# Kernel tuning notes

Measured on AMD Instinct MI355X. Metric: run time of the kernel, lower is better.

The kernel has to match this reference:

```python
import jax, jax.numpy as jnp
import numpy as np

D_MODEL = 1024
N_HEADS = 16
HEAD_DIM = 64
SEQ = 2048
BATCH = 2
NEG = -1e9


def rotate_half(t):
    t1, t2 = jnp.split(t, 2, axis=-1)
    return jnp.concatenate([-t2, t1], axis=-1)


def setup_inputs() -> dict:
    key = jax.random.key(0)
    ks = jax.random.split(key, 7)
    std = 0.02
    x = jax.random.normal(ks[0], (BATCH, SEQ, D_MODEL), dtype=jnp.float32)
    # RoPE tables [seq_len, head_dim]
    inv_freq = 1.0 / (10000.0 ** (jnp.arange(0, HEAD_DIM, 2, dtype=jnp.float32) / HEAD_DIM))
    t = jnp.arange(SEQ, dtype=jnp.float32)
    freqs = jnp.outer(t, inv_freq)
    emb = jnp.concatenate([freqs, freqs], axis=-1)
    cos = jnp.cos(emb)
    sin = jnp.sin(emb)
    Wq = std * jax.random.normal(ks[1], (D_MODEL, D_MODEL), dtype=jnp.float32)
    Wk = std * jax.random.normal(ks[2], (D_MODEL, D_MODEL), dtype=jnp.float32)
    Wv = std * jax.random.normal(ks[3], (D_MODEL, D_MODEL), dtype=jnp.float32)
    Wo = std * jax.random.normal(ks[4], (D_MODEL, D_MODEL), dtype=jnp.float32)
    return {"x": x, "cos": cos, "sin": sin, "Wq": Wq, "Wk": Wk, "Wv": Wv, "Wo": Wo}


def reference(x, cos, sin, Wq, Wk, Wv, Wo):
    B, S, _ = x.shape
    scale = 1.0 / np.sqrt(HEAD_DIM)
    # projections (nn.Linear: y = x @ W.T)
    q = (x @ Wq.T).reshape(B, S, N_HEADS, HEAD_DIM).transpose(0, 2, 1, 3)  # [B,H,S,D]
    k = (x @ Wk.T).reshape(B, S, N_HEADS, HEAD_DIM).transpose(0, 2, 1, 3)
    v = (x @ Wv.T).reshape(B, S, N_HEADS, HEAD_DIM).transpose(0, 2, 1, 3)
    # RoPE
    c = cos[None, None, :, :]
    s = sin[None, None, :, :]
    q = q * c + rotate_half(q) * s
    k = k * c + rotate_half(k) * s
    # attention with additive causal mask
    scores = jnp.einsum('bhqd,bhkd->bhqk', q, k) * scale
    causal = jnp.triu(jnp.ones((S, S), dtype=jnp.float32), k=1) * NEG
    scores = scores + causal[None, None]
    attn = jax.nn.softmax(scores, axis=-1)
    out = jnp.einsum('bhqk,bhkd->bhqd', attn, v)
    out = out.transpose(0, 2, 1, 3).reshape(B, S, D_MODEL)
    return out @ Wo.T
```

## Files before the change

### kernel.cpp

```cpp
#include <hip/hip_runtime.h>
#include <hip/hip_bf16.h>
#include <math.h>

#define DM    1024
#define SEQL  2048
#define NB    2
#define MTOT  4096

typedef __attribute__((ext_vector_type(8))) short short8;
typedef __attribute__((ext_vector_type(4))) short short4v;
typedef __attribute__((ext_vector_type(4))) float float4v;

#define GLDS16(g, l) __builtin_amdgcn_global_load_lds( \
    (const __attribute__((address_space(1))) void*)(g), \
    (__attribute__((address_space(3))) void*)(l), 16, 0, 0)

__device__ __forceinline__ short f2bf(float f) {
  union { float f; unsigned u; } c; c.f = f;
  unsigned r = c.u + 0x7FFFu + ((c.u >> 16) & 1u);
  return (short)(r >> 16);
}

__device__ __forceinline__ int packbf(float a, float b) {
  union { float f; unsigned u; } ca, cb; ca.f = a; cb.f = b;
  return (int)__builtin_amdgcn_perm(cb.u + 0x8000u, ca.u + 0x8000u, 0x07060302u);
}

__global__ __launch_bounds__(256) void cvt_all(
    const float* __restrict__ x, const float* __restrict__ wq, const float* __restrict__ wk,
    const float* __restrict__ wv, const float* __restrict__ wo,
    short* __restrict__ xb, short* __restrict__ wqb, short* __restrict__ wkb,
    short* __restrict__ wvb, short* __restrict__ wob) {
  const int n4x = MTOT * DM / 4;
  int i = blockIdx.x * 256 + threadIdx.x;
  const float* s; short* d; int off;
  if (i < n4x) { s = x; d = xb; off = i; }
  else {
    int j = i - n4x;
    int sel = j >> 18;
    off = j & 0x3FFFF;
    s = (sel == 0) ? wq : (sel == 1) ? wk : (sel == 2) ? wv : wo;
    d = (sel == 0) ? wqb : (sel == 1) ? wkb : (sel == 2) ? wvb : wob;
  }
  float4 v = ((const float4*)s)[off];
  short4v o;
  o.x = f2bf(v.x); o.y = f2bf(v.y); o.z = f2bf(v.z); o.w = f2bf(v.w);
  ((short4v*)d)[off] = o;
}

__global__ __launch_bounds__(256, 2) void qkv_kernel(
    const short* __restrict__ A,
    const short* __restrict__ B0, const short* __restrict__ B1, const short* __restrict__ B2,
    short* __restrict__ out0, short* __restrict__ out1, short* __restrict__ out2,
    const float* __restrict__ cosp, const float* __restrict__ sinp)
{
  __shared__ short As[3][128 * 32];
  __shared__ short Bs[3][3][64 * 32];
  const int t = threadIdx.x;
  const int w = t >> 6, lane = t & 63;
  const int quad = lane >> 4, l16 = lane & 15;
  const int bm = blockIdx.y * 128, bn = blockIdx.x * 64;

  const short* Bz[3] = { B0, B1, B2 };

  float4v acc[3][2][4];
#pragma unroll
  for (int z = 0; z < 3; ++z)
#pragma unroll
    for (int i = 0; i < 2; ++i)
#pragma unroll
      for (int j = 0; j < 4; ++j) { float4v zr = {0.f, 0.f, 0.f, 0.f}; acc[z][i][j] = zr; }

  auto stage = [&](int k0, int p) {
#pragma unroll
    for (int i = 0; i < 2; ++i) {
      const int s = i * 256 + t;
      const int row = s >> 2, kc = (s & 3) ^ (row & 3);
      GLDS16(A + (size_t)(bm + row) * DM + k0 + kc * 8, &As[p][(i * 256 + w * 64) * 8]);
    }
#pragma unroll
    for (int z = 0; z < 3; ++z) {
      const int row = t >> 2, kc = (t & 3) ^ (row & 3);
      GLDS16(Bz[z] + (size_t)(bn + row) * DM + k0 + kc * 8, &Bs[z][p][(w * 64) * 8]);
    }
  };

  stage(0, 0);
  stage(32, 1);
  for (int ki = 0; ki < 32; ++ki) {
    const int p = ki % 3;
    if (ki < 31) { asm volatile("s_waitcnt vmcnt(5)" ::: "memory"); }
    else         { asm volatile("s_waitcnt vmcnt(0)" ::: "memory"); }
    __builtin_amdgcn_s_barrier();
    __builtin_amdgcn_sched_barrier(0);
    if (ki + 2 < 32) stage((ki + 2) * 32, (ki + 2) % 3);

    short8 af[2], bf[3][4];
#pragma unroll
    for (int mt = 0; mt < 2; ++mt) {
      const int row = w * 32 + mt * 16 + l16;
      af[mt] = *(const short8*)&As[p][(row * 4 + (quad ^ (row & 3))) * 8];
    }
#pragma unroll
    for (int z = 0; z < 3; ++z)
#pragma unroll
      for (int nt = 0; nt < 4; ++nt) {
        const int row = nt * 16 + l16;
        bf[z][nt] = *(const short8*)&Bs[z][p][(row * 4 + (quad ^ (row & 3))) * 8];
      }
    __builtin_amdgcn_s_setprio(1);
#pragma unroll
    for (int z = 0; z < 3; ++z)
#pragma unroll
      for (int mt = 0; mt < 2; ++mt)
#pragma unroll
        for (int nt = 0; nt < 4; ++nt)
          acc[z][mt][nt] = __builtin_amdgcn_mfma_f32_16x16x32_bf16(
              af[mt], bf[z][nt], acc[z][mt][nt], 0, 0, 0);
    __builtin_amdgcn_s_setprio(0);
  }

#pragma unroll
  for (int z = 0; z < 2; ++z) {
    short* qo = (z == 0) ? out0 : out1;
    const float sc = (z == 0) ? 0.18033688011112042f : 1.0f;
#pragma unroll
    for (int mt = 0; mt < 2; ++mt)
#pragma unroll
      for (int r = 0; r < 4; ++r) {
        int grow = bm + w * 32 + mt * 16 + quad * 4 + r;
        int s = grow & (SEQL - 1);
        int base = grow * DM + bn;
#pragma unroll
        for (int nt = 0; nt < 2; ++nt) {
          int d1 = nt * 16 + l16;
          float q1 = acc[z][mt][nt][r], q2 = acc[z][mt][nt + 2][r];
          float c1 = cosp[s * 64 + d1] * sc,      s1 = sinp[s * 64 + d1] * sc;
          float c2 = cosp[s * 64 + 32 + d1] * sc, s2 = sinp[s * 64 + 32 + d1] * sc;
          qo[base + d1]      = f2bf(q1 * c1 - q2 * s1);
          qo[base + 32 + d1] = f2bf(q2 * c2 + q1 * s2);
        }
      }
  }
#pragma unroll
  for (int mt = 0; mt < 2; ++mt)
#pragma unroll
    for (int nt = 0; nt < 4; ++nt) {
      int gc = bn + nt * 16 + l16;
      int g0 = bm + w * 32 + mt * 16 + quad * 4;
      short4v pk;
#pragma unroll
      for (int r = 0; r < 4; ++r) pk[r] = f2bf(acc[2][mt][nt][r]);
      *(short4v*)&out2[(size_t)gc * MTOT + g0] = pk;
    }
}

__global__ __launch_bounds__(512, 4) void attn_kernel(
    const short* __restrict__ Q, const short* __restrict__ K,
    const short* __restrict__ Vt, short* __restrict__ O)
{
  __shared__ short smem[34816];
  short* Ks = smem;
  short* Vs = smem + 8192;
  const int t = threadIdx.x;
  const int wid = t >> 6, lane = t & 63;
  const int quad = lane >> 4, l16 = lane & 15;
  const int g = wid >> 2;
  const int qg = wid & 3;
  short* Pl = smem + 16384 + wid * (2 * 16 * 72);
  const int qtA = blockIdx.x, qtB = 31 - blockIdx.x;
  const int bh = blockIdx.y, b = bh >> 4, h = bh & 15;
  const int rowbase = b * SEQL, colbase = h * 64;
  const int nktA = (qtA >> 1) + 1, nktB = (qtB >> 1) + 1;
  const int qA = qtA * 64 + qg * 16 + l16;
  const int qB = qtB * 64 + qg * 16 + l16;

  short8 aqA[2], aqB[2];
#pragma unroll
  for (int kk = 0; kk < 2; ++kk) {
    aqA[kk] = *(const short8*)&Q[(size_t)(rowbase + qA) * DM + colbase + kk * 32 + quad * 8];
    aqB[kk] = *(const short8*)&Q[(size_t)(rowbase + qB) * DM + colbase + kk * 32 + quad * 8];
  }

  float4v oA[4], oB[4];
#pragma unroll
  for (int j = 0; j < 4; ++j) { float4v z = {0.f, 0.f, 0.f, 0.f}; oA[j] = z; oB[j] = z; }
  float lA = 0.f, lB = 0.f;

  const short* Kbase0 = K + (size_t)rowbase * DM + colbase;
  const short* Vbase0 = Vt + (size_t)colbase * MTOT + rowbase;

  auto stageK = [&](int kt) {
#pragma unroll
    for (int j = 0; j < 2; ++j) {
      int i = j * 512 + t;
      int n = i >> 3, c = (i & 7) ^ (n & 7);
      GLDS16(Kbase0 + (size_t)(kt * 128 + n) * DM + c * 8, Ks + (j * 512 + wid * 64) * 8);
    }
  };
  auto stageV = [&](int kt) {
#pragma unroll
    for (int j = 0; j < 2; ++j) {
      int i = j * 512 + t;
      int d = i >> 4, c = (i & 15) ^ (d & 7);
      GLDS16(Vbase0 + (size_t)d * MTOT + kt * 128 + c * 8, Vs + (j * 512 + wid * 64) * 8);
    }
  };

  stageK(0);
  stageV(0);
  for (int kt = 0; kt < nktB; ++kt) {
    asm volatile("s_waitcnt vmcnt(2)" ::: "memory");
    __builtin_amdgcn_s_barrier();
    __builtin_amdgcn_sched_barrier(0);

    const bool actA = (kt < nktA);
    const bool diagA = (kt == nktA - 1), diagB = (kt == nktB - 1);

#pragma unroll
    for (int ntl = 0; ntl < 4; ++ntl) {
      const int nt = g * 4 + ntl;
      const int n = nt * 16 + l16;
      short8 bk0 = *(const short8*)&Ks[(n * 8 + (quad ^ (n & 7))) * 8];
      short8 bk1 = *(const short8*)&Ks[(n * 8 + ((4 + quad) ^ (n & 7))) * 8];
      const int kb = kt * 128 + nt * 16 + quad * 4;
      float4v zz = {0.f, 0.f, 0.f, 0.f};
      __builtin_amdgcn_s_setprio(1);
      float4v sB = __builtin_amdgcn_mfma_f32_16x16x32_bf16(bk0, aqB[0], zz, 0, 0, 0);
      sB = __builtin_amdgcn_mfma_f32_16x16x32_bf16(bk1, aqB[1], sB, 0, 0, 0);
      float4v sA;
      if (actA) {
        sA = __builtin_amdgcn_mfma_f32_16x16x32_bf16(bk0, aqA[0], zz, 0, 0, 0);
        sA = __builtin_amdgcn_mfma_f32_16x16x32_bf16(bk1, aqA[1], sA, 0, 0, 0);
      }
      __builtin_amdgcn_s_setprio(0);
      float pb[4];
#pragma unroll
      for (int r = 0; r < 4; ++r) {
        float pv = (diagB && (kb + r > qB)) ? 0.f : __builtin_amdgcn_exp2f(sB[r]);
        lB += pv; pb[r] = pv;
      }
      *(int2*)&Pl[1 * 16 * 72 + l16 * 72 + ntl * 16 + quad * 4] =
          make_int2(packbf(pb[0], pb[1]), packbf(pb[2], pb[3]));
      if (actA) {
        float pa[4];
#pragma unroll
        for (int r = 0; r < 4; ++r) {
          float pv = (diagA && (kb + r > qA)) ? 0.f : __builtin_amdgcn_exp2f(sA[r]);
          lA += pv; pa[r] = pv;
        }
        *(int2*)&Pl[0 * 16 * 72 + l16 * 72 + ntl * 16 + quad * 4] =
            make_int2(packbf(pa[0], pa[1]), packbf(pa[2], pa[3]));
      }
    }

    asm volatile("s_waitcnt vmcnt(0)" ::: "memory");
    __builtin_amdgcn_s_barrier();
    __builtin_amdgcn_sched_barrier(0);

    if (kt + 1 < nktB) stageK(kt + 1);

#pragma unroll
    for (int kk = 0; kk < 2; ++kk) {
      short8 apB = *(const short8*)&Pl[1 * 16 * 72 + l16 * 72 + kk * 32 + quad * 8];
      short8 apA;
      if (actA) apA = *(const short8*)&Pl[0 * 16 * 72 + l16 * 72 + kk * 32 + quad * 8];
      const int c0 = g * 8 + kk * 4 + quad;
      __builtin_amdgcn_s_setprio(1);
#pragma unroll
      for (int dt = 0; dt < 4; ++dt) {
        const int d = dt * 16 + l16;
        short8 bv = *(const short8*)&Vs[(d * 16 + (c0 ^ (d & 7))) * 8];
        oB[dt] = __builtin_amdgcn_mfma_f32_16x16x32_bf16(apB, bv, oB[dt], 0, 0, 0);
        if (actA) oA[dt] = __builtin_amdgcn_mfma_f32_16x16x32_bf16(apA, bv, oA[dt], 0, 0, 0);
      }
      __builtin_amdgcn_s_setprio(0);
    }

    __builtin_amdgcn_s_barrier();
    __builtin_amdgcn_sched_barrier(0);

    if (kt + 1 < nktB) stageV(kt + 1);
  }

  lA += __shfl_xor(lA, 16); lA += __shfl_xor(lA, 32);
  lB += __shfl_xor(lB, 16); lB += __shfl_xor(lB, 32);

  __syncthreads();
  float* Ored = (float*)smem;
  float* Lred = (float*)smem + 8448;
  if (g == 1) {
#pragma unroll
    for (int tile = 0; tile < 2; ++tile) {
      const float4v* src = (tile == 0) ? oA : oB;
      const int base = ((tile * 4 + qg) * 16) * 66;
#pragma unroll
      for (int dt = 0; dt < 4; ++dt)
#pragma unroll
        for (int r = 0; r < 4; ++r)
          Ored[base + (quad * 4 + r) * 66 + dt * 16 + l16] = src[dt][r];
    }
    if (lane < 16) {
      Lred[(0 * 4 + qg) * 16 + l16] = lA;
      Lred[(1 * 4 + qg) * 16 + l16] = lB;
    }
  }
  __syncthreads();
  if (g == 0) {
    const float tA = lA + Lred[(0 * 4 + qg) * 16 + l16];
    const float tB = lB + Lred[(1 * 4 + qg) * 16 + l16];
    float iAr[4], iBr[4];
#pragma unroll
    for (int r = 0; r < 4; ++r) {
      iAr[r] = 1.f / __shfl(tA, quad * 4 + r);
      iBr[r] = 1.f / __shfl(tB, quad * 4 + r);
    }
#pragma unroll
    for (int tile = 0; tile < 2; ++tile) {
      const float4v* src = (tile == 0) ? oA : oB;
      const int qt = (tile == 0) ? qtA : qtB;
      const int base = ((tile * 4 + qg) * 16) * 66;
#pragma unroll
      for (int dt = 0; dt < 4; ++dt)
#pragma unroll
        for (int r = 0; r < 4; ++r) {
          float v = src[dt][r] + Ored[base + (quad * 4 + r) * 66 + dt * 16 + l16];
          int grow = rowbase + qt * 64 + qg * 16 + quad * 4 + r;
          int gcol = colbase + dt * 16 + l16;
          O[(size_t)grow * DM + gcol] = f2bf(v * ((tile == 0) ? iAr[r] : iBr[r]));
        }
    }
  }
}

__global__ __launch_bounds__(256, 2) void gemm_out(
    const short* __restrict__ A, const short* __restrict__ B,
    float* __restrict__ out)
{
  __shared__ short As[3][128 * 32];
  __shared__ short Bs[3][64 * 32];
  const int t = threadIdx.x;
  const int w = t >> 6, lane = t & 63;
  const int quad = lane >> 4, l16 = lane & 15;
  const int wm = w >> 1, wn = w & 1;
  const int bm = blockIdx.y * 128, bn = blockIdx.x * 64;

  float4v acc[4][2];
#pragma unroll
  for (int i = 0; i < 4; ++i)
#pragma unroll
    for (int j = 0; j < 2; ++j) { float4v z = {0.f, 0.f, 0.f, 0.f}; acc[i][j] = z; }

  auto stage = [&](int k0, int p) {
#pragma unroll
    for (int i = 0; i < 2; ++i) {
      const int row = (i * 256 + t) >> 2, kc = (i * 256 + t) & 3;
      GLDS16(A + (size_t)(bm + row) * DM + k0 + kc * 8, &As[p][(i * 256 + w * 64) * 8]);
    }
    {
      const int row = t >> 2, kc = t & 3;
      GLDS16(B + (size_t)(bn + row) * DM + k0 + kc * 8, &Bs[p][(w * 64) * 8]);
    }
  };

  stage(0, 0);
  stage(32, 1);
  for (int ki = 0; ki < 32; ++ki) {
    const int p = ki % 3;
    if (ki < 31) { asm volatile("s_waitcnt vmcnt(3)" ::: "memory"); }
    else         { asm volatile("s_waitcnt vmcnt(0)" ::: "memory"); }
    __builtin_amdgcn_s_barrier();
    __builtin_amdgcn_sched_barrier(0);
    if (ki + 2 < 32) stage((ki + 2) * 32, (ki + 2) % 3);
    short8 af[4], bf[2];
#pragma unroll
    for (int mt = 0; mt < 4; ++mt) af[mt] = *(const short8*)&As[p][(wm * 64 + mt * 16 + l16) * 32 + quad * 8];
#pragma unroll
    for (int nt = 0; nt < 2; ++nt) bf[nt] = *(const short8*)&Bs[p][(wn * 32 + nt * 16 + l16) * 32 + quad * 8];
#pragma unroll
    for (int mt = 0; mt < 4; ++mt)
#pragma unroll
      for (int nt = 0; nt < 2; ++nt)
        acc[mt][nt] = __builtin_amdgcn_mfma_f32_16x16x32_bf16(af[mt], bf[nt], acc[mt][nt], 0, 0, 0);
  }

#pragma unroll
  for (int mt = 0; mt < 4; ++mt)
#pragma unroll
    for (int nt = 0; nt < 2; ++nt)
#pragma unroll
      for (int r = 0; r < 4; ++r) {
        int grow = bm + wm * 64 + mt * 16 + quad * 4 + r;
        int gcol = bn + wn * 32 + nt * 16 + l16;
        out[(size_t)grow * DM + gcol] = acc[mt][nt][r];
      }
}

extern "C" void kernel_launch(void* const* d_in, const int* in_sizes, int n_in,
                              void* d_out, int out_size, void* d_ws, size_t ws_size,
                              hipStream_t stream) {
  const float* x    = (const float*)d_in[0];
  const float* cosp = (const float*)d_in[1];
  const float* sinp = (const float*)d_in[2];
  const float* Wq   = (const float*)d_in[3];
  const float* Wk   = (const float*)d_in[4];
  const float* Wv   = (const float*)d_in[5];
  const float* Wo   = (const float*)d_in[6];

  char* ws = (char*)d_ws;
  const size_t XB = (size_t)MTOT * DM * 2;
  const size_t WB = (size_t)DM * DM * 2;
  short* xb    = (short*)(ws);
  short* wqb   = (short*)(ws + XB);
  short* wkb   = (short*)(ws + XB + 1 * WB);
  short* wvb   = (short*)(ws + XB + 2 * WB);
  short* wob   = (short*)(ws + XB + 3 * WB);
  short* Qb    = (short*)(ws + XB + 4 * WB);
  short* Kb    = (short*)(ws + XB + 4 * WB + XB);
  short* Vtb   = (short*)(ws + XB + 4 * WB + 2 * XB);
  short* attnb = xb;

  const int n4tot = (MTOT * DM + 4 * DM * DM) / 4;
  hipLaunchKernelGGL(cvt_all, dim3(n4tot / 256), dim3(256), 0, stream,
                     x, Wq, Wk, Wv, Wo, xb, wqb, wkb, wvb, wob);

  hipLaunchKernelGGL(qkv_kernel, dim3(DM / 64, MTOT / 128), dim3(256), 0, stream,
                     xb, wqb, wkb, wvb, Qb, Kb, Vtb, cosp, sinp);

  hipLaunchKernelGGL(attn_kernel, dim3(16, NB * 16), dim3(512), 0, stream,
                     Qb, Kb, Vtb, attnb);

  hipLaunchKernelGGL(gemm_out, dim3(DM / 64, MTOT / 128), dim3(256), 0, stream,
                     attnb, wob, (float*)d_out);
}
```

Baseline: 180.8 us.

## Fuse fp32-to-bf16 conversion into QKV GEMM and drop separate convert kernel

Removes the standalone cvt_all launch and makes the QKV projection kernel read fp32 x and weights directly, converting to bf16 in registers and writing swizzled tiles to LDS with double buffering instead of a triple-buffered direct global-to-LDS path. The Wo conversion is appended to the tail of the QKV kernel, one 2048-element chunk per block. This saves a kernel launch and the extra round trip through bf16 workspace copies. In exchange the GEMM loads twice the bytes per tile through registers, adds conversion ALU work and VGPR pressure inside the main loop, and loses the async global-to-LDS prefetch depth.

```diff
diff --git a/kernel.cpp b/kernel.cpp
--- a/kernel.cpp
+++ b/kernel.cpp
@@ -26,42 +26,59 @@
   return (int)__builtin_amdgcn_perm(cb.u + 0x8000u, ca.u + 0x8000u, 0x07060302u);
 }
 
-__global__ __launch_bounds__(256) void cvt_all(
-    const float* __restrict__ x, const float* __restrict__ wq, const float* __restrict__ wk,
-    const float* __restrict__ wv, const float* __restrict__ wo,
-    short* __restrict__ xb, short* __restrict__ wqb, short* __restrict__ wkb,
-    short* __restrict__ wvb, short* __restrict__ wob) {
-  const int n4x = MTOT * DM / 4;
-  int i = blockIdx.x * 256 + threadIdx.x;
-  const float* s; short* d; int off;
-  if (i < n4x) { s = x; d = xb; off = i; }
-  else {
-    int j = i - n4x;
-    int sel = j >> 18;
-    off = j & 0x3FFFF;
-    s = (sel == 0) ? wq : (sel == 1) ? wk : (sel == 2) ? wv : wo;
-    d = (sel == 0) ? wqb : (sel == 1) ? wkb : (sel == 2) ? wvb : wob;
-  }
-  float4 v = ((const float4*)s)[off];
-  short4v o;
-  o.x = f2bf(v.x); o.y = f2bf(v.y); o.z = f2bf(v.z); o.w = f2bf(v.w);
-  ((short4v*)d)[off] = o;
-}
-
 __global__ __launch_bounds__(256, 2) void qkv_kernel(
-    const short* __restrict__ A,
-    const short* __restrict__ B0, const short* __restrict__ B1, const short* __restrict__ B2,
+    const float* __restrict__ X,
+    const float* __restrict__ W0, const float* __restrict__ W1, const float* __restrict__ W2,
+    const float* __restrict__ Wo,
     short* __restrict__ out0, short* __restrict__ out1, short* __restrict__ out2,
+    short* __restrict__ wob,
     const float* __restrict__ cosp, const float* __restrict__ sinp)
 {
-  __shared__ short As[3][128 * 32];
-  __shared__ short Bs[3][3][64 * 32];
+  __shared__ short As[2][128 * 32];
+  __shared__ short Bs[2][3][64 * 32];
   const int t = threadIdx.x;
   const int w = t >> 6, lane = t & 63;
   const int quad = lane >> 4, l16 = lane & 15;
   const int bm = blockIdx.y * 128, bn = blockIdx.x * 64;
-
-  const short* Bz[3] = { B0, B1, B2 };
+  const float* Wz[3] = { W0, W1, W2 };
+
+  const int arow = t >> 1, ah = t & 1;
+  const int wrow = t >> 2, wq4 = t & 3;
+
+  float4 a4[4];
+  float4 w4[3][2];
+
+  auto loads = [&](int k0) {
+    const float* ap = X + (size_t)(bm + arow) * DM + k0 + ah * 16;
+#pragma unroll
+    for (int i = 0; i < 4; ++i) a4[i] = ((const float4*)ap)[i];
+#pragma unroll
+    for (int z = 0; z < 3; ++z) {
+      const float* wp = Wz[z] + (size_t)(bn + wrow) * DM + k0 + wq4 * 8;
+#pragma unroll
+      for (int i = 0; i < 2; ++i) w4[z][i] = ((const float4*)wp)[i];
+    }
+  };
+  auto cvtwrite = [&](int p) {
+#pragma unroll
+    for (int j = 0; j < 2; ++j) {
+      float4 u = a4[2 * j], v = a4[2 * j + 1];
+      short8 s;
+      s[0] = f2bf(u.x); s[1] = f2bf(u.y); s[2] = f2bf(u.z); s[3] = f2bf(u.w);
+      s[4] = f2bf(v.x); s[5] = f2bf(v.y); s[6] = f2bf(v.z); s[7] = f2bf(v.w);
+      const int cs = (ah * 2 + j) ^ ((arow >> 1) & 3);
+      *(short8*)&As[p][(arow * 4 + cs) * 8] = s;
+    }
+#pragma unroll
+    for (int z = 0; z < 3; ++z) {
+      float4 u = w4[z][0], v = w4[z][1];
+      short8 s;
+      s[0] = f2bf(u.x); s[1] = f2bf(u.y); s[2] = f2bf(u.z); s[3] = f2bf(u.w);
+      s[4] = f2bf(v.x); s[5] = f2bf(v.y); s[6] = f2bf(v.z); s[7] = f2bf(v.w);
+      const int cs = wq4 ^ ((wrow >> 1) & 3);
+      *(short8*)&Bs[p][z][(wrow * 4 + cs) * 8] = s;
+    }
+  };
 
   float4v acc[3][2][4];
 #pragma unroll
@@ -71,42 +88,29 @@
 #pragma unroll
       for (int j = 0; j < 4; ++j) { float4v zr = {0.f, 0.f, 0.f, 0.f}; acc[z][i][j] = zr; }
 
-  auto stage = [&](int k0, int p) {
-#pragma unroll
-    for (int i = 0; i < 2; ++i) {
-      const int s = i * 256 + t;
-      const int row = s >> 2, kc = (s & 3) ^ (row & 3);
-      GLDS16(A + (size_t)(bm + row) * DM + k0 + kc * 8, &As[p][(i * 256 + w * 64) * 8]);
-    }
-#pragma unroll
-    for (int z = 0; z < 3; ++z) {
-      const int row = t >> 2, kc = (t & 3) ^ (row & 3);
-      GLDS16(Bz[z] + (size_t)(bn + row) * DM + k0 + kc * 8, &Bs[z][p][(w * 64) * 8]);
-    }
-  };
-
-  stage(0, 0);
-  stage(32, 1);
+  loads(0);
+  cvtwrite(0);
+
   for (int ki = 0; ki < 32; ++ki) {
-    const int p = ki % 3;
-    if (ki < 31) { asm volatile("s_waitcnt vmcnt(5)" ::: "memory"); }
-    else         { asm volatile("s_waitcnt vmcnt(0)" ::: "memory"); }
+    const int p = ki & 1;
+    asm volatile("s_waitcnt lgkmcnt(0)" ::: "memory");
     __builtin_amdgcn_s_barrier();
     __builtin_amdgcn_sched_barrier(0);
-    if (ki + 2 < 32) stage((ki + 2) * 32, (ki + 2) % 3);
+    if (ki + 1 < 32) loads((ki + 1) * 32);
+    __builtin_amdgcn_sched_barrier(0);
 
     short8 af[2], bf[3][4];
 #pragma unroll
     for (int mt = 0; mt < 2; ++mt) {
       const int row = w * 32 + mt * 16 + l16;
-      af[mt] = *(const short8*)&As[p][(row * 4 + (quad ^ (row & 3))) * 8];
+      af[mt] = *(const short8*)&As[p][(row * 4 + (quad ^ ((row >> 1) & 3))) * 8];
     }
 #pragma unroll
     for (int z = 0; z < 3; ++z)
 #pragma unroll
       for (int nt = 0; nt < 4; ++nt) {
         const int row = nt * 16 + l16;
-        bf[z][nt] = *(const short8*)&Bs[z][p][(row * 4 + (quad ^ (row & 3))) * 8];
+        bf[z][nt] = *(const short8*)&Bs[p][z][(row * 4 + (quad ^ ((row >> 1) & 3))) * 8];
       }
     __builtin_amdgcn_s_setprio(1);
 #pragma unroll
@@ -118,6 +122,7 @@
           acc[z][mt][nt] = __builtin_amdgcn_mfma_f32_16x16x32_bf16(
               af[mt], bf[z][nt], acc[z][mt][nt], 0, 0, 0);
     __builtin_amdgcn_s_setprio(0);
+    if (ki + 1 < 32) cvtwrite(p ^ 1);
   }
 
 #pragma unroll
@@ -153,6 +158,17 @@
       for (int r = 0; r < 4; ++r) pk[r] = f2bf(acc[2][mt][nt][r]);
       *(short4v*)&out2[(size_t)gc * MTOT + g0] = pk;
     }
+
+  {
+    const int bid = blockIdx.y * 16 + blockIdx.x;
+    const size_t base = (size_t)bid * 2048 + t * 8;
+    float4 u = ((const float4*)(Wo + base))[0];
+    float4 v = ((const float4*)(Wo + base))[1];
+    short8 s;
+    s[0] = f2bf(u.x); s[1] = f2bf(u.y); s[2] = f2bf(u.z); s[3] = f2bf(u.w);
+    s[4] = f2bf(v.x); s[5] = f2bf(v.y); s[6] = f2bf(v.z); s[7] = f2bf(v.w);
+    *(short8*)&wob[base] = s;
+  }
 }
 
 __global__ __launch_bounds__(512, 4) void attn_kernel(
@@ -410,22 +426,14 @@
   char* ws = (char*)d_ws;
   const size_t XB = (size_t)MTOT * DM * 2;
   const size_t WB = (size_t)DM * DM * 2;
-  short* xb    = (short*)(ws);
-  short* wqb   = (short*)(ws + XB);
-  short* wkb   = (short*)(ws + XB + 1 * WB);
-  short* wvb   = (short*)(ws + XB + 2 * WB);
   short* wob   = (short*)(ws + XB + 3 * WB);
   short* Qb    = (short*)(ws + XB + 4 * WB);
   short* Kb    = (short*)(ws + XB + 4 * WB + XB);
   short* Vtb   = (short*)(ws + XB + 4 * WB + 2 * XB);
-  short* attnb = xb;
-
-  const int n4tot = (MTOT * DM + 4 * DM * DM) / 4;
-  hipLaunchKernelGGL(cvt_all, dim3(n4tot / 256), dim3(256), 0, stream,
-                     x, Wq, Wk, Wv, Wo, xb, wqb, wkb, wvb, wob);
+  short* attnb = (short*)(ws);
 
   hipLaunchKernelGGL(qkv_kernel, dim3(DM / 64, MTOT / 128), dim3(256), 0, stream,
-                     xb, wqb, wkb, wvb, Qb, Kb, Vtb, cosp, sinp);
+                     x, Wq, Wk, Wv, Wo, Qb, Kb, Vtb, wob, cosp, sinp);
 
   hipLaunchKernelGGL(attn_kernel, dim3(16, NB * 16), dim3(512), 0, stream,
                      Qb, Kb, Vtb, attnb);
```

Result: slower. 213.0 us (+17.8%).
